# Kernel optimization log

Measured on AMD Instinct MI355X. Metric: run time of the kernel, lower is better.

Reference implementation:

```python
import jax, jax.numpy as jnp
import numpy as np

NUM_EXPERTS = 8
TOP_K = 2


def setup_inputs() -> dict:
    key = jax.random.key(0)
    ks = jax.random.split(key, 5)
    B, S, H, F, E = 4, 2048, 1024, 4096, NUM_EXPERTS
    scale_h = 1.0 / np.sqrt(H)
    scale_f = 1.0 / np.sqrt(F)
    return {
        "hidden_states": jax.random.normal(ks[0], (B, S, H), dtype=jnp.float32),
        "Wr": jax.random.normal(ks[1], (H, E), dtype=jnp.float32) * scale_h,
        "br": jnp.zeros((E,), dtype=jnp.float32),
        "W1": jax.random.normal(ks[2], (E, H, F), dtype=jnp.float32) * scale_h,
        "b1": jnp.zeros((E, F), dtype=jnp.float32),
        "W2": jax.random.normal(ks[3], (E, F, H), dtype=jnp.float32) * scale_f,
        "b2": jnp.zeros((E, H), dtype=jnp.float32),
    }


def _moe_forward(x, Wr, br, W1, b1, W2, b2):
    B, S, H = x.shape
    T = B * S
    xf = x.reshape(T, H)
    # Router: softmax over expert logits, take top-k, renormalize weights.
    logits = xf @ Wr + br                      # [T, E]
    probs = jax.nn.softmax(logits, axis=-1)
    top_p, top_i = jax.lax.top_k(probs, TOP_K)  # [T, K]
    weights = top_p / jnp.sum(top_p, axis=-1, keepdims=True)
    # combine[t, e] = sum_k weights[t,k] * (top_i[t,k] == e)
    one_hot = jax.nn.one_hot(top_i, NUM_EXPERTS, dtype=xf.dtype)  # [T, K, E]
    combine = jnp.einsum("tk,tke->te", weights, one_hot)          # [T, E]
    # Per-expert FFN (loop over small fixed expert count); weighted sum.
    out = jnp.zeros_like(xf)
    for e in range(NUM_EXPERTS):
        h = jax.nn.gelu(xf @ W1[e] + b1[e], approximate=False)    # [T, F]
        y = h @ W2[e] + b2[e]                                     # [T, H]
        out = out + combine[:, e:e + 1] * y
    return out.reshape(B, S, H)


def reference(hidden_states, Wr, br, W1, b1, W2, b2):
    return _moe_forward(hidden_states, Wr, br, W1, b1, W2, b2)
```

## Files before the change

### kernel.cpp

```cpp
#include <hip/hip_runtime.h>
#include <cstdint>
#include <cmath>

#define T_TOK 8192
#define H_DIM 1024
#define F_DIM 4096
#define NE 8
#define CAP 8192
#define BK 64
#define BM 128
#define BN1 128
#define BN2 128
#define MBLK 32
#define LDK 140
#define RTOK 32

typedef __attribute__((ext_vector_type(8))) short short8v;
typedef __attribute__((ext_vector_type(4))) float f32x4;

static __device__ __forceinline__ unsigned short f2bf(float f) {
    union { float f; unsigned int u; } v; v.f = f;
    unsigned int r = v.u + 0x7FFFu + ((v.u >> 16) & 1u);
    return (unsigned short)(r >> 16);
}

static __device__ __forceinline__ float bf2f(unsigned short u) {
    union { unsigned int i; float f; } v; v.i = ((unsigned)u) << 16; return v.f;
}

static __device__ __forceinline__ float fast_gelu(float x) {
    const float s  = x * 0.70710678118f;
    const float as = fabsf(s);
    const float t  = __builtin_amdgcn_rcpf(fmaf(0.3275911f, as, 1.f));
    float p = fmaf(1.061405429f, t, -1.453152027f);
    p = fmaf(p, t, 1.421413741f);
    p = fmaf(p, t, -0.284496736f);
    p = fmaf(p, t, 0.254829592f);
    p = p * t;
    const float E = __expf(-as * as);
    const float erf_abs = fmaf(-p, E, 1.f);
    const float erf_s = copysignf(erf_abs, s);
    return 0.5f * x * (1.f + erf_s);
}

static __device__ __forceinline__ void gl_lds16(const void* g, void* l) {
    __builtin_amdgcn_global_load_lds(
        (const __attribute__((address_space(1))) unsigned int*)g,
        (__attribute__((address_space(3))) unsigned int*)l, 16, 0, 0);
}

static __device__ __forceinline__ int prefix128(const int* cnt, int e) {
    int o = 0;
    for (int q = 0; q < e; ++q) o += ((cnt[q] + 127) >> 7) << 7;
    return o;
}

static __device__ __forceinline__ void transpose_tile(
    const float* __restrict__ in, unsigned short* __restrict__ out,
    int R, int C, int e, int bx, int by, unsigned short* tile_s)
{
    const int r0 = by * 128, c0 = bx * 64;
    const int colg = threadIdx.x & 15;
    const int rowg = threadIdx.x >> 4;
    const float* ip = in + (size_t)e * R * C + (size_t)r0 * C + c0;
#pragma unroll
    for (int p = 0; p < 2; ++p) {
        const int rr = (rowg + p * 16) * 4;
        const float4 v0 = *(const float4*)(ip + (size_t)(rr + 0) * C + colg * 4);
        const float4 v1 = *(const float4*)(ip + (size_t)(rr + 1) * C + colg * 4);
        const float4 v2 = *(const float4*)(ip + (size_t)(rr + 2) * C + colg * 4);
        const float4 v3 = *(const float4*)(ip + (size_t)(rr + 3) * C + colg * 4);
        const float rv[4][4] = {{v0.x, v0.y, v0.z, v0.w}, {v1.x, v1.y, v1.z, v1.w},
                                {v2.x, v2.y, v2.z, v2.w}, {v3.x, v3.y, v3.z, v3.w}};
#pragma unroll
        for (int ci = 0; ci < 4; ++ci) {
            ushort4 o;
            o.x = f2bf(rv[0][ci]); o.y = f2bf(rv[1][ci]);
            o.z = f2bf(rv[2][ci]); o.w = f2bf(rv[3][ci]);
            *(ushort4*)(tile_s + (colg * 4 + ci) * LDK + rr) = o;
        }
    }
    __syncthreads();
    unsigned short* op = out + (size_t)e * R * C + (size_t)c0 * R + r0;
#pragma unroll
    for (int p = 0; p < 4; ++p) {
        const int c = (threadIdx.x >> 4) + p * 16;
        const int s = (threadIdx.x & 15) * 8;
        const unsigned short* sp = tile_s + c * LDK + s;
        const uint2 w0 = *(const uint2*)(sp);
        const uint2 w1 = *(const uint2*)(sp + 4);
        uint4 o4; o4.x = w0.x; o4.y = w0.y; o4.z = w1.x; o4.w = w1.y;
        *(uint4*)(op + (size_t)c * R + s) = o4;
    }
}

#define G_ROUT (T_TOK / RTOK)
#define G_TC   4096

__global__ __launch_bounds__(256) void prep_k(
    const float* __restrict__ x, const float* __restrict__ Wr,
    const float* __restrict__ br,
    const float* __restrict__ W1, const float* __restrict__ W2,
    int* __restrict__ cnt, int* __restrict__ perm,
    int* __restrict__ inv, float* __restrict__ tw,
    unsigned short* __restrict__ xb,
    unsigned short* __restrict__ w1t, unsigned short* __restrict__ w2t)
{
    __shared__ __align__(16) unsigned short tile_s[64 * LDK];
    __shared__ int   sh_e01[RTOK];
    __shared__ float sh_w0[RTOK];
    __shared__ int   sh_r0[RTOK], sh_r1[RTOK];
    __shared__ int   lcnt[NE], gbase[NE];
    const int bid = blockIdx.x;
    const int tid = threadIdx.x;

    if (bid >= G_ROUT) {
        if (bid < G_ROUT + G_TC) {
            const int j = bid - G_ROUT;
            const int e = j >> 9; const int rem = j & 511;
            transpose_tile(W1, w1t, H_DIM, F_DIM, e, rem >> 3, rem & 7, tile_s);
        } else {
            const int j = bid - G_ROUT - G_TC;
            const int e = j >> 9; const int rem = j & 511;
            transpose_tile(W2, w2t, F_DIM, H_DIM, e, rem >> 5, rem & 31, tile_s);
        }
        return;
    }

    const int wave = tid >> 6;
    const int lane = tid & 63;
    if (tid < NE) lcnt[tid] = 0;
    __syncthreads();

    for (int tk = 0; tk < RTOK / 4; ++tk) {
        const int li = wave * (RTOK / 4) + tk;
        const int t = bid * RTOK + li;
        const float* xr = x + (size_t)t * H_DIM;
        float acc[NE];
#pragma unroll
        for (int e = 0; e < NE; ++e) acc[e] = 0.f;
#pragma unroll
        for (int c0 = 0; c0 < H_DIM; c0 += 256) {
            const float4 v = *(const float4*)(xr + c0 + lane * 4);
            ushort4 ob;
            ob.x = f2bf(v.x); ob.y = f2bf(v.y); ob.z = f2bf(v.z); ob.w = f2bf(v.w);
            *(ushort4*)(xb + (size_t)t * H_DIM + c0 + lane * 4) = ob;
            const int hbase = c0 + lane * 4;
            float vv[4] = {v.x, v.y, v.z, v.w};
#pragma unroll
            for (int i = 0; i < 4; ++i) {
                const float4 w0 = *(const float4*)(Wr + (size_t)(hbase + i) * NE);
                const float4 w1 = *(const float4*)(Wr + (size_t)(hbase + i) * NE + 4);
                acc[0] += vv[i] * w0.x; acc[1] += vv[i] * w0.y;
                acc[2] += vv[i] * w0.z; acc[3] += vv[i] * w0.w;
                acc[4] += vv[i] * w1.x; acc[5] += vv[i] * w1.y;
                acc[6] += vv[i] * w1.z; acc[7] += vv[i] * w1.w;
            }
        }
#pragma unroll
        for (int off = 32; off > 0; off >>= 1) {
#pragma unroll
            for (int e = 0; e < NE; ++e) acc[e] += __shfl_xor(acc[e], off, 64);
        }
        if (lane == 0) {
#pragma unroll
            for (int e = 0; e < NE; ++e) acc[e] += br[e];
            int i0 = 0; float l0 = acc[0];
#pragma unroll
            for (int e = 1; e < NE; ++e) if (acc[e] > l0) { l0 = acc[e]; i0 = e; }
            int i1 = -1; float l1 = -3.4e38f;
#pragma unroll
            for (int e = 0; e < NE; ++e) if (e != i0 && acc[e] > l1) { l1 = acc[e]; i1 = e; }
            sh_e01[li] = (i0 << 3) | i1;
            sh_w0[li] = 1.f / (1.f + expf(l1 - l0));
        }
    }
    __syncthreads();

    if (tid < RTOK) {
        const int e0 = sh_e01[tid] >> 3, e1 = sh_e01[tid] & 7;
        sh_r0[tid] = atomicAdd(&lcnt[e0], 1);
        sh_r1[tid] = atomicAdd(&lcnt[e1], 1);
    }
    __syncthreads();
    if (tid < NE) gbase[tid] = atomicAdd(&cnt[tid], lcnt[tid]);
    __syncthreads();
    if (tid < RTOK) {
        const int t = bid * RTOK + tid;
        const int e0 = sh_e01[tid] >> 3, e1 = sh_e01[tid] & 7;
        const int p0 = gbase[e0] + sh_r0[tid];
        const int p1 = gbase[e1] + sh_r1[tid];
        const float w0 = sh_w0[tid];
        perm[e0 * CAP + p0] = t;
        perm[e1 * CAP + p1] = t;
        inv[2 * t + 0] = (e0 << 13) | p0;  tw[2 * t + 0] = w0;
        inv[2 * t + 1] = (e1 << 13) | p1;  tw[2 * t + 1] = 1.f - w0;
    }
}

__global__ __launch_bounds__(256, 2) void gemm1_k(
    const unsigned short* __restrict__ xb,
    const unsigned short* __restrict__ w1t,
    const float* __restrict__ b1,
    unsigned short* __restrict__ hbuf,
    const int* __restrict__ perm, const int* __restrict__ cnt)
{
    __shared__ __align__(16) unsigned short smem[(BM + BN1) * BK];
    __shared__ int rows_s[BM];

    constexpr int NY = F_DIM / BN1;
    constexpr int nwg = MBLK * NY * NE;
    const int bid = blockIdx.x;
    const int wg = (bid & 7) * (nwg >> 3) + (bid >> 3);
    const int e  = wg / (MBLK * NY);
    const int rem = wg % (MBLK * NY);
    const int nb = rem / MBLK;
    const int mb = rem % MBLK;

    const int c = cnt[e];
    const int m0 = mb * BM;
    if (m0 >= c) return;
    const int tid = threadIdx.x;

    if (tid < BM) {
        const int i = m0 + tid;
        rows_s[tid] = perm[e * CAP + (i < c ? i : c - 1)];
    }
    __syncthreads();

    const int lane = tid & 63;
    const int w = tid >> 6;
    const int srow = tid >> 3;
    const int u = tid & 7;
    const int us = (u ^ (srow & 7)) * 8;

    const unsigned short* bp = w1t + ((size_t)e * F_DIM + nb * BN1) * H_DIM;
    const unsigned short* srcA[4];
    const unsigned short* srcB[4];
    int dstA[4], dstB[4];
#pragma unroll
    for (int j = 0; j < 4; ++j) {
        srcA[j] = xb + (size_t)rows_s[j * 32 + srow] * H_DIM + us;
        dstA[j] = (j * 32 + w * 8) * BK + lane * 8;
        srcB[j] = bp + (size_t)(j * 32 + srow) * H_DIM + us;
        dstB[j] = BM * BK + dstA[j];
    }

    f32x4 acc[4][4];
#pragma unroll
    for (int m = 0; m < 4; ++m)
#pragma unroll
        for (int n = 0; n < 4; ++n) acc[m][n] = (f32x4){0.f, 0.f, 0.f, 0.f};

    const int wr = (tid >> 7) & 1;
    const int wc = (tid >> 6) & 1;
    const int fr = lane & 15;
    const int fg = lane >> 4;
    const int fx = fr & 7;

    for (int k0 = 0; k0 < H_DIM; k0 += BK) {
#pragma unroll
        for (int j = 0; j < 4; ++j) gl_lds16(srcA[j] + k0, smem + dstA[j]);
#pragma unroll
        for (int j = 0; j < 4; ++j) gl_lds16(srcB[j] + k0, smem + dstB[j]);
        __syncthreads();
        const unsigned short* A = smem;
        const unsigned short* B = smem + BM * BK;
#pragma unroll
        for (int kk = 0; kk < 2; ++kk) {
            const int q = kk * 4 + fg;
            const int ua = (q ^ fx) * 8;
            short8v a[4], b[4];
#pragma unroll
            for (int m = 0; m < 4; ++m)
                a[m] = *(const short8v*)(A + (wr * 64 + m * 16 + fr) * BK + ua);
#pragma unroll
            for (int n = 0; n < 4; ++n)
                b[n] = *(const short8v*)(B + (wc * 64 + n * 16 + fr) * BK + ua);
#pragma unroll
            for (int m = 0; m < 4; ++m)
#pragma unroll
                for (int n = 0; n < 4; ++n)
                    acc[m][n] = __builtin_amdgcn_mfma_f32_16x16x32_bf16(b[n], a[m], acc[m][n], 0, 0, 0);
        }
        __syncthreads();
    }

    const size_t hrow0 = (size_t)prefix128(cnt, e) + m0;
#pragma unroll
    for (int n = 0; n < 4; ++n) {
        const int f = nb * BN1 + wc * 64 + n * 16 + fg * 4;
        const float4 bv = *(const float4*)(b1 + e * F_DIM + f);
        const float bb[4] = {bv.x, bv.y, bv.z, bv.w};
#pragma unroll
        for (int m = 0; m < 4; ++m) {
            const int tl = wr * 64 + m * 16 + fr;
            ushort4 o;
#pragma unroll
            for (int r = 0; r < 4; ++r) {
                const float g = fast_gelu(acc[m][n][r] + bb[r]);
                ((unsigned short*)&o)[r] = f2bf(g);
            }
            *(ushort4*)(hbuf + (hrow0 + tl) * F_DIM + f) = o;
        }
    }
}

__global__ __launch_bounds__(256, 2) void gemm2_k(
    const unsigned short* __restrict__ hbuf,
    const unsigned short* __restrict__ w2t,
    const float* __restrict__ b2,
    unsigned short* __restrict__ ybuf,
    const int* __restrict__ cnt)
{
    __shared__ __align__(16) unsigned short smem[(BM + BN2) * BK];

    constexpr int NY = H_DIM / BN2;
    constexpr int nwg = MBLK * NY * NE;
    const int bid = blockIdx.x;
    const int wg = (bid & 7) * (nwg >> 3) + (bid >> 3);
    const int e  = wg / (MBLK * NY);
    const int rem = wg % (MBLK * NY);
    const int nb = rem / MBLK;
    const int mb = rem % MBLK;

    const int c = cnt[e];
    const int m0 = mb * BM;
    if (m0 >= c) return;
    const int tid = threadIdx.x;

    const int lane = tid & 63;
    const int w = tid >> 6;
    const int srow = tid >> 3;
    const int u = tid & 7;
    const int us = (u ^ (srow & 7)) * 8;

    const size_t arow0 = (size_t)prefix128(cnt, e) + m0;
    const unsigned short* bp = w2t + ((size_t)e * H_DIM + nb * BN2) * F_DIM;
    const unsigned short* srcA[4];
    const unsigned short* srcB[4];
    int dstA[4], dstB[4];
#pragma unroll
    for (int j = 0; j < 4; ++j) {
        srcA[j] = hbuf + (arow0 + j * 32 + srow) * F_DIM + us;
        dstA[j] = (j * 32 + w * 8) * BK + lane * 8;
        srcB[j] = bp + (size_t)(j * 32 + srow) * F_DIM + us;
        dstB[j] = BM * BK + dstA[j];
    }

    f32x4 acc[4][4];
#pragma unroll
    for (int m = 0; m < 4; ++m)
#pragma unroll
        for (int n = 0; n < 4; ++n) acc[m][n] = (f32x4){0.f, 0.f, 0.f, 0.f};

    const int wr = (tid >> 7) & 1;
    const int wc = (tid >> 6) & 1;
    const int fr = lane & 15;
    const int fg = lane >> 4;
    const int fx = fr & 7;

    for (int k0 = 0; k0 < F_DIM; k0 += BK) {
#pragma unroll
        for (int j = 0; j < 4; ++j) gl_lds16(srcA[j] + k0, smem + dstA[j]);
#pragma unroll
        for (int j = 0; j < 4; ++j) gl_lds16(srcB[j] + k0, smem + dstB[j]);
        __syncthreads();
        const unsigned short* A = smem;
        const unsigned short* B = smem + BM * BK;
#pragma unroll
        for (int kk = 0; kk < 2; ++kk) {
            const int q = kk * 4 + fg;
            const int ua = (q ^ fx) * 8;
            short8v a[4], b[4];
#pragma unroll
            for (int m = 0; m < 4; ++m)
                a[m] = *(const short8v*)(A + (wr * 64 + m * 16 + fr) * BK + ua);
#pragma unroll
            for (int n = 0; n < 4; ++n)
                b[n] = *(const short8v*)(B + (wc * 64 + n * 16 + fr) * BK + ua);
#pragma unroll
            for (int m = 0; m < 4; ++m)
#pragma unroll
                for (int n = 0; n < 4; ++n)
                    acc[m][n] = __builtin_amdgcn_mfma_f32_16x16x32_bf16(b[n], a[m], acc[m][n], 0, 0, 0);
        }
        __syncthreads();
    }

#pragma unroll
    for (int n = 0; n < 4; ++n) {
        const int h = nb * BN2 + wc * 64 + n * 16 + fg * 4;
        const float4 bv = *(const float4*)(b2 + e * H_DIM + h);
#pragma unroll
        for (int m = 0; m < 4; ++m) {
            const int tl = wr * 64 + m * 16 + fr;
            ushort4 o;
            o.x = f2bf(acc[m][n][0] + bv.x);
            o.y = f2bf(acc[m][n][1] + bv.y);
            o.z = f2bf(acc[m][n][2] + bv.z);
            o.w = f2bf(acc[m][n][3] + bv.w);
            *(ushort4*)(ybuf + (arow0 + tl) * H_DIM + h) = o;
        }
    }
}

__global__ __launch_bounds__(256) void combine_k(
    const unsigned short* __restrict__ ybuf, const int* __restrict__ inv,
    const float* __restrict__ tw, const int* __restrict__ cnt,
    float* __restrict__ out)
{
    const int t = blockIdx.x;
    const int j = threadIdx.x;
    const int i0 = inv[2 * t], i1 = inv[2 * t + 1];
    const float w0 = tw[2 * t], w1 = tw[2 * t + 1];
    const size_t r0 = (size_t)prefix128(cnt, i0 >> 13) + (i0 & 8191);
    const size_t r1 = (size_t)prefix128(cnt, i1 >> 13) + (i1 & 8191);
    const ushort4 a = *(const ushort4*)(ybuf + r0 * H_DIM + j * 4);
    const ushort4 b = *(const ushort4*)(ybuf + r1 * H_DIM + j * 4);
    float4 o;
    o.x = w0 * bf2f(a.x) + w1 * bf2f(b.x);
    o.y = w0 * bf2f(a.y) + w1 * bf2f(b.y);
    o.z = w0 * bf2f(a.z) + w1 * bf2f(b.z);
    o.w = w0 * bf2f(a.w) + w1 * bf2f(b.w);
    *(float4*)(out + (size_t)t * H_DIM + j * 4) = o;
}

extern "C" void kernel_launch(void* const* d_in, const int* in_sizes, int n_in,
                              void* d_out, int out_size, void* d_ws, size_t ws_size,
                              hipStream_t stream)
{
    const float* x  = (const float*)d_in[0];
    const float* Wr = (const float*)d_in[1];
    const float* br = (const float*)d_in[2];
    const float* W1 = (const float*)d_in[3];
    const float* b1 = (const float*)d_in[4];
    const float* W2 = (const float*)d_in[5];
    const float* b2 = (const float*)d_in[6];
    float* out = (float*)d_out;

    char* ws = (char*)d_ws;
    size_t off = 0;
    auto alloc = [&](size_t bytes) {
        char* p = ws + off;
        off += (bytes + 255) & ~(size_t)255;
        return p;
    };
    unsigned short* w2t  = (unsigned short*)alloc((size_t)NE * H_DIM * F_DIM * 2);
    unsigned short* w1t  = (unsigned short*)alloc((size_t)NE * F_DIM * H_DIM * 2);
    unsigned short* xb   = (unsigned short*)alloc((size_t)T_TOK * H_DIM * 2);
    unsigned short* hbuf = (unsigned short*)alloc((size_t)(T_TOK * 2 + NE * BM) * F_DIM * 2);
    int*   cnt  = (int*)alloc(NE * 4);
    int*   perm = (int*)alloc((size_t)NE * CAP * 4);
    int*   inv  = (int*)alloc((size_t)T_TOK * 2 * 4);
    float* tw   = (float*)alloc((size_t)T_TOK * 2 * 4);
    unsigned short* ybuf = w1t;
    (void)ws_size; (void)in_sizes; (void)n_in; (void)out_size;

    hipMemsetAsync(cnt, 0, NE * 4, stream);
    prep_k<<<G_ROUT + 2 * G_TC, 256, 0, stream>>>(x, Wr, br, W1, W2,
                                                  cnt, perm, inv, tw, xb, w1t, w2t);
    gemm1_k<<<MBLK * (F_DIM / BN1) * NE, 256, 0, stream>>>(xb, w1t, b1, hbuf, perm, cnt);
    gemm2_k<<<MBLK * (H_DIM / BN2) * NE, 256, 0, stream>>>(hbuf, w2t, b2, ybuf, cnt);
    combine_k<<<T_TOK, 256, 0, stream>>>(ybuf, inv, tw, cnt, out);
}
```

Baseline: 480.0 us.

## Enlarge gemm1 M-tile to 256 rows with 512-thread blocks

The first expert GEMM now uses 256-token tiles computed by 8 waves of 512 threads, so each W1 tile loaded into LDS serves twice as many token rows. Expert segment padding in the hidden and output buffers is raised to a 256-row granularity, and gemm2 and the combine kernel use the new offsets. This cuts W1 traffic and load instructions per FLOP, but LDS use per block grows, padding waste per expert increases, and tiles with few valid rows still do full work.

```diff
diff --git a/kernel.cpp b/kernel.cpp
--- a/kernel.cpp
+++ b/kernel.cpp
@@ -8,9 +8,11 @@
 #define NE 8
 #define CAP 8192
 #define BK 64
+#define BM1 256
 #define BM 128
 #define BN1 128
 #define BN2 128
+#define MBLK1 16
 #define MBLK 32
 #define LDK 140
 #define RTOK 32
@@ -49,9 +51,9 @@
         (__attribute__((address_space(3))) unsigned int*)l, 16, 0, 0);
 }
 
-static __device__ __forceinline__ int prefix128(const int* cnt, int e) {
+static __device__ __forceinline__ int prefix256(const int* cnt, int e) {
     int o = 0;
-    for (int q = 0; q < e; ++q) o += ((cnt[q] + 127) >> 7) << 7;
+    for (int q = 0; q < e; ++q) o += ((cnt[q] + 255) >> 8) << 8;
     return o;
 }
 
@@ -198,31 +200,31 @@
     }
 }
 
-__global__ __launch_bounds__(256, 2) void gemm1_k(
+__global__ __launch_bounds__(512, 2) void gemm1_k(
     const unsigned short* __restrict__ xb,
     const unsigned short* __restrict__ w1t,
     const float* __restrict__ b1,
     unsigned short* __restrict__ hbuf,
     const int* __restrict__ perm, const int* __restrict__ cnt)
 {
-    __shared__ __align__(16) unsigned short smem[(BM + BN1) * BK];
-    __shared__ int rows_s[BM];
+    __shared__ __align__(16) unsigned short smem[(BM1 + BN1) * BK];
+    __shared__ int rows_s[BM1];
 
     constexpr int NY = F_DIM / BN1;
-    constexpr int nwg = MBLK * NY * NE;
+    constexpr int nwg = MBLK1 * NY * NE;
     const int bid = blockIdx.x;
     const int wg = (bid & 7) * (nwg >> 3) + (bid >> 3);
-    const int e  = wg / (MBLK * NY);
-    const int rem = wg % (MBLK * NY);
-    const int nb = rem / MBLK;
-    const int mb = rem % MBLK;
+    const int e  = wg / (MBLK1 * NY);
+    const int rem = wg % (MBLK1 * NY);
+    const int nb = rem / MBLK1;
+    const int mb = rem % MBLK1;
 
     const int c = cnt[e];
-    const int m0 = mb * BM;
+    const int m0 = mb * BM1;
     if (m0 >= c) return;
     const int tid = threadIdx.x;
 
-    if (tid < BM) {
+    if (tid < BM1) {
         const int i = m0 + tid;
         rows_s[tid] = perm[e * CAP + (i < c ? i : c - 1)];
     }
@@ -235,15 +237,14 @@
     const int us = (u ^ (srow & 7)) * 8;
 
     const unsigned short* bp = w1t + ((size_t)e * F_DIM + nb * BN1) * H_DIM;
-    const unsigned short* srcA[4];
-    const unsigned short* srcB[4];
-    int dstA[4], dstB[4];
-#pragma unroll
-    for (int j = 0; j < 4; ++j) {
-        srcA[j] = xb + (size_t)rows_s[j * 32 + srow] * H_DIM + us;
-        dstA[j] = (j * 32 + w * 8) * BK + lane * 8;
-        srcB[j] = bp + (size_t)(j * 32 + srow) * H_DIM + us;
-        dstB[j] = BM * BK + dstA[j];
+    const unsigned short* src[6];
+    int dst[6];
+#pragma unroll
+    for (int j = 0; j < 6; ++j) {
+        const int r = j * 64 + srow;
+        src[j] = (j < 4) ? (xb + (size_t)rows_s[r] * H_DIM + us)
+                         : (bp + (size_t)(r - BM1) * H_DIM + us);
+        dst[j] = (j * 64 + w * 8) * BK + lane * 8;
     }
 
     f32x4 acc[4][4];
@@ -252,20 +253,18 @@
 #pragma unroll
         for (int n = 0; n < 4; ++n) acc[m][n] = (f32x4){0.f, 0.f, 0.f, 0.f};
 
-    const int wr = (tid >> 7) & 1;
-    const int wc = (tid >> 6) & 1;
+    const int wq = w & 3;
+    const int wn = w >> 2;
     const int fr = lane & 15;
     const int fg = lane >> 4;
     const int fx = fr & 7;
 
     for (int k0 = 0; k0 < H_DIM; k0 += BK) {
 #pragma unroll
-        for (int j = 0; j < 4; ++j) gl_lds16(srcA[j] + k0, smem + dstA[j]);
-#pragma unroll
-        for (int j = 0; j < 4; ++j) gl_lds16(srcB[j] + k0, smem + dstB[j]);
+        for (int j = 0; j < 6; ++j) gl_lds16(src[j] + k0, smem + dst[j]);
         __syncthreads();
         const unsigned short* A = smem;
-        const unsigned short* B = smem + BM * BK;
+        const unsigned short* B = smem + BM1 * BK;
 #pragma unroll
         for (int kk = 0; kk < 2; ++kk) {
             const int q = kk * 4 + fg;
@@ -273,10 +272,10 @@
             short8v a[4], b[4];
 #pragma unroll
             for (int m = 0; m < 4; ++m)
-                a[m] = *(const short8v*)(A + (wr * 64 + m * 16 + fr) * BK + ua);
+                a[m] = *(const short8v*)(A + (wq * 64 + m * 16 + fr) * BK + ua);
 #pragma unroll
             for (int n = 0; n < 4; ++n)
-                b[n] = *(const short8v*)(B + (wc * 64 + n * 16 + fr) * BK + ua);
+                b[n] = *(const short8v*)(B + (wn * 64 + n * 16 + fr) * BK + ua);
 #pragma unroll
             for (int m = 0; m < 4; ++m)
 #pragma unroll
@@ -286,15 +285,15 @@
         __syncthreads();
     }
 
-    const size_t hrow0 = (size_t)prefix128(cnt, e) + m0;
+    const size_t hrow0 = (size_t)prefix256(cnt, e) + m0;
 #pragma unroll
     for (int n = 0; n < 4; ++n) {
-        const int f = nb * BN1 + wc * 64 + n * 16 + fg * 4;
+        const int f = nb * BN1 + wn * 64 + n * 16 + fg * 4;
         const float4 bv = *(const float4*)(b1 + e * F_DIM + f);
         const float bb[4] = {bv.x, bv.y, bv.z, bv.w};
 #pragma unroll
         for (int m = 0; m < 4; ++m) {
-            const int tl = wr * 64 + m * 16 + fr;
+            const int tl = wq * 64 + m * 16 + fr;
             ushort4 o;
 #pragma unroll
             for (int r = 0; r < 4; ++r) {
@@ -335,7 +334,7 @@
     const int u = tid & 7;
     const int us = (u ^ (srow & 7)) * 8;
 
-    const size_t arow0 = (size_t)prefix128(cnt, e) + m0;
+    const size_t arow0 = (size_t)prefix256(cnt, e) + m0;
     const unsigned short* bp = w2t + ((size_t)e * H_DIM + nb * BN2) * F_DIM;
     const unsigned short* srcA[4];
     const unsigned short* srcB[4];
@@ -414,8 +413,8 @@
     const int j = threadIdx.x;
     const int i0 = inv[2 * t], i1 = inv[2 * t + 1];
     const float w0 = tw[2 * t], w1 = tw[2 * t + 1];
-    const size_t r0 = (size_t)prefix128(cnt, i0 >> 13) + (i0 & 8191);
-    const size_t r1 = (size_t)prefix128(cnt, i1 >> 13) + (i1 & 8191);
+    const size_t r0 = (size_t)prefix256(cnt, i0 >> 13) + (i0 & 8191);
+    const size_t r1 = (size_t)prefix256(cnt, i1 >> 13) + (i1 & 8191);
     const ushort4 a = *(const ushort4*)(ybuf + r0 * H_DIM + j * 4);
     const ushort4 b = *(const ushort4*)(ybuf + r1 * H_DIM + j * 4);
     float4 o;
@@ -449,7 +448,7 @@
     unsigned short* w2t  = (unsigned short*)alloc((size_t)NE * H_DIM * F_DIM * 2);
     unsigned short* w1t  = (unsigned short*)alloc((size_t)NE * F_DIM * H_DIM * 2);
     unsigned short* xb   = (unsigned short*)alloc((size_t)T_TOK * H_DIM * 2);
-    unsigned short* hbuf = (unsigned short*)alloc((size_t)(T_TOK * 2 + NE * BM) * F_DIM * 2);
+    unsigned short* hbuf = (unsigned short*)alloc((size_t)(T_TOK * 2 + NE * BM1) * F_DIM * 2);
     int*   cnt  = (int*)alloc(NE * 4);
     int*   perm = (int*)alloc((size_t)NE * CAP * 4);
     int*   inv  = (int*)alloc((size_t)T_TOK * 2 * 4);
@@ -460,7 +459,7 @@
     hipMemsetAsync(cnt, 0, NE * 4, stream);
     prep_k<<<G_ROUT + 2 * G_TC, 256, 0, stream>>>(x, Wr, br, W1, W2,
                                                   cnt, perm, inv, tw, xb, w1t, w2t);
-    gemm1_k<<<MBLK * (F_DIM / BN1) * NE, 256, 0, stream>>>(xb, w1t, b1, hbuf, perm, cnt);
+    gemm1_k<<<MBLK1 * (F_DIM / BN1) * NE, 512, 0, stream>>>(xb, w1t, b1, hbuf, perm, cnt);
     gemm2_k<<<MBLK * (H_DIM / BN2) * NE, 256, 0, stream>>>(hbuf, w2t, b2, ybuf, cnt);
     combine_k<<<T_TOK, 256, 0, stream>>>(ybuf, inv, tw, cnt, out);
 }
```

Result: slower. 507.3 us (+5.7%).
